# Kernel optimization log

Hardware: AMD Instinct MI355X
Metric: run time of the kernel (lower is better)

## Reference

```python
import jax, jax.numpy as jnp
import numpy as np
from jax import lax

LAP = jnp.array([[1.0, 2.0, 1.0], [2.0, -12.0, 2.0], [1.0, 2.0, 1.0]], jnp.float32)
SOBEL_X = jnp.array([[-1.0, 0.0, 1.0], [-2.0, 0.0, 2.0], [-1.0, 0.0, 1.0]], jnp.float32)

GENE_SIZE = 3
UPDATE_RATE = 0.5
LEAKY_SLOPE = 0.01  # torch leaky_relu default


def _depthwise3x3_circular(x, k):
    # x: [B,C,H,W], k: [3,3]; circular pad then depthwise conv with same kernel per channel
    b, c, h, w = x.shape
    xp = jnp.pad(x, ((0, 0), (0, 0), (1, 1), (1, 1)), mode='wrap')
    kern = jnp.broadcast_to(k, (c, 1, 3, 3))
    return lax.conv_general_dilated(
        xp, kern, window_strides=(1, 1), padding='VALID',
        dimension_numbers=('NCHW', 'OIHW', 'NCHW'), feature_group_count=c)


def setup_inputs() -> dict:
    key = jax.random.key(0)
    k1, k2, k3, k4, k5 = jax.random.split(key, 5)
    chn, hidden_n, gene_size = 12, 128, 3
    perc_n = 3 * chn  # 36
    b, h, w = 16, 256, 256
    return {
        'x': jax.random.normal(k1, (b, chn, h, w), jnp.float32),
        'rand': jax.random.uniform(k2, (b, 1, h, w), jnp.float32),
        'w1_w': jax.random.normal(k3, (hidden_n, perc_n), jnp.float32) * 0.1,
        'w1_b': jax.random.normal(k4, (hidden_n,), jnp.float32) * 0.1,
        'w2_w': jax.random.normal(k5, (chn - gene_size, hidden_n), jnp.float32) * 0.1,
    }


def reference(x, rand, w1_w, w1_b, w2_w):
    b, c, h, w = x.shape
    gene = x[:, -GENE_SIZE:]
    # perception: ident (=x) and laplacian interleaved per channel, then gradient norm
    gx = _depthwise3x3_circular(x, SOBEL_X)
    gy = _depthwise3x3_circular(x, SOBEL_X.T)
    lap_x = _depthwise3x3_circular(x, LAP)
    state_lap = jnp.stack([x, lap_x], axis=2).reshape(b, 2 * c, h, w)  # [x0,lap0,x1,lap1,...]
    gradnorm = jnp.sqrt(gx * gx + gy * gy + 1e-8)
    perc = jnp.concatenate([state_lap, gradnorm], axis=1)  # [B, 3C, H, W]
    # 1x1 conv MLP
    y = jnp.einsum('bchw,oc->bohw', perc, w1_w) + w1_b[None, :, None, None]
    y = jax.nn.leaky_relu(y, LEAKY_SLOPE)
    y = jnp.einsum('bchw,oc->bohw', y, w2_w)  # [B, C-gene, H, W]
    # stochastic update mask
    update_mask = jnp.floor(rand + UPDATE_RATE)  # [B,1,H,W]
    # alive mask: 3x3 max pool (torch pads with -inf) on channel 3
    pool = lax.reduce_window(x[:, 3], -jnp.inf, lax.max,
                             (1, 3, 3), (1, 1, 1), [(0, 0), (1, 1), (1, 1)])
    life = (pool > 0.1)[:, None].astype(x.dtype)  # [B,1,H,W]
    x_new = x[:, :c - GENE_SIZE] + y * update_mask * life
    return jnp.concatenate([x_new, gene], axis=1)
```

## Files before the change

kernel.cpp:

```cpp
#include <hip/hip_runtime.h>
#include <hip/hip_bf16.h>
#include <math.h>

#define CHN  12
#define H    256
#define W    256
#define HID  128
#define OUTC 9
#define PSTR 56
#define YSTR 72

typedef __attribute__((ext_vector_type(4))) float    f32x4;
typedef __attribute__((ext_vector_type(8))) short    s16x8;
typedef __attribute__((ext_vector_type(4))) unsigned u32x4;
typedef __attribute__((ext_vector_type(8))) __bf16   bf16x8;

#define MFMA16x16x32(a, b, c) \
    __builtin_amdgcn_mfma_f32_16x16x32_bf16(__builtin_bit_cast(bf16x8, (a)), \
                                            __builtin_bit_cast(bf16x8, (b)), (c), 0, 0, 0)

static __device__ __forceinline__ unsigned short bfbits(float f) {
    __hip_bfloat16 h = __float2bfloat16(f);
    return __builtin_bit_cast(unsigned short, h);
}
static __device__ __forceinline__ float bits2f(unsigned short u) {
    __hip_bfloat16 h = __builtin_bit_cast(__hip_bfloat16, u);
    return __bfloat162float(h);
}
static __device__ __forceinline__ unsigned rna(float f) {
    return __builtin_bit_cast(unsigned, f) + 0x8000u;
}
static __device__ __forceinline__ unsigned pack2(unsigned uodd, unsigned ueven) {
    return __builtin_amdgcn_perm(uodd, ueven, 0x07060302u);
}
static __device__ __forceinline__ float fast_sqrtf(float x) {
    float r;
    asm("v_sqrt_f32 %0, %1" : "=v"(r) : "v"(x));
    return r;
}

__global__ void prep_weights(const float* __restrict__ w1w, const float* __restrict__ w1b,
                             const float* __restrict__ w2w, unsigned short* __restrict__ wsbuf)
{
    const int t = threadIdx.x;
    const int l = t & 63;
    const int grp = t >> 6;
    const int row = l & 15;
    const int g4 = l >> 4;
    unsigned short* wsa1 = wsbuf;
    unsigned short* wsa2 = wsbuf + 16 * 64 * 8;

    for (int mf = grp; mf < 16; mf += 4) {
        int m = mf >> 1, f = mf & 1;
        int hid = m * 16 + row;
        for (int j = 0; j < 8; ++j) {
            int s = f * 32 + g4 * 8 + j;
            unsigned short v = 0;
            if (s < 36)       v = bfbits(w1w[hid * 36 + s]);
            else if (s < 48)  v = bfbits(w1w[hid * 36 + 2 * (s - 36) + 1]);
            else if (s == 48) v = bfbits(w1b[hid]);
            wsa1[(mf * 64 + l) * 8 + j] = v;
        }
    }
    {
        int kb = grp;
        for (int j = 0; j < 8; ++j) {
            float wv = (row < OUTC) ? w2w[row * HID + kb * 32 + g4 * 8 + j] : 0.f;
            wsa2[(kb * 64 + l) * 8 + j] = bfbits(wv);
        }
    }
}

__global__ __launch_bounds__(256, 3) void nca_main(
    const float* __restrict__ x, const float* __restrict__ rnd,
    const unsigned short* __restrict__ wsbuf, float* __restrict__ out)
{
    union SMem {
        struct { float2 csdd[CHN][W]; float prrow[W]; } s;
        unsigned short perc[W][PSTR];
    };
    __shared__ SMem sm;
    __shared__ unsigned short y1h[4][16][YSTR];

    const int t = threadIdx.x;
    const int orig = ((blockIdx.x & 7) << 9) | (blockIdx.x >> 3);
    const int h = orig & (H - 1);
    const int b = orig >> 8;
    const int hm = (h + H - 1) & (H - 1);
    const int hp = (h + 1) & (H - 1);
    const float* xb = x + (size_t)b * CHN * H * W;

    float xc[CHN], csr[CHN], ddr[CHN];
    const float maskraw = rnd[((size_t)b * H + h) * W + t];
    #pragma unroll
    for (int c = 0; c < CHN; ++c) {
        const float* xp = xb + (size_t)c * H * W;
        float v0 = xp[hm * W + t];
        float v1 = xp[h  * W + t];
        float v2 = xp[hp * W + t];
        xc[c] = v1;
        float cs = fmaf(2.f, v1, v0) + v2;
        float dd = v2 - v0;
        csr[c] = cs; ddr[c] = dd;
        sm.s.csdd[c][t] = make_float2(cs, dd);
        if (c == 3) {
            float cm = v1;
            if (h > 0)     cm = fmaxf(cm, v0);
            if (h < H - 1) cm = fmaxf(cm, v2);
            sm.s.prrow[t] = cm;
        }
    }
    __syncthreads();

    const int wm = (t + W - 1) & (W - 1);
    const int wp = (t + 1) & (W - 1);
    float perc[36];
    #pragma unroll
    for (int c = 0; c < CHN; ++c) {
        float2 vm = sm.s.csdd[c][wm];
        float2 vp = sm.s.csdd[c][wp];
        float gx  = vp.x - vm.x;
        float gy  = fmaf(2.f, ddr[c], vm.y) + vp.y;
        float lap = fmaf(2.f, csr[c], vm.x + vp.x) - 16.f * xc[c];
        perc[2 * c]     = xc[c];
        perc[2 * c + 1] = lap;
        perc[24 + c]    = fast_sqrtf(fmaf(gx, gx, gy * gy) + 1e-8f);
    }
    float scale_reg;
    {
        float pool = sm.s.prrow[t];
        if (t > 0)     pool = fmaxf(pool, sm.s.prrow[wm]);
        if (t < W - 1) pool = fmaxf(pool, sm.s.prrow[wp]);
        scale_reg = (pool > 0.1f && maskraw >= 0.5f) ? 1.f : 0.f;
    }
    const float gene0 = xc[9], gene1 = xc[10], gene2 = xc[11];
    __syncthreads();

    {
        unsigned u[48];
        #pragma unroll
        for (int s = 0; s < 36; ++s) u[s] = rna(perc[s]);
        #pragma unroll
        for (int k = 0; k < 12; ++k) {
            float hif = __builtin_bit_cast(float, u[2 * k + 1] & 0xFFFF0000u);
            u[36 + k] = rna(perc[2 * k + 1] - hif);
        }
        unsigned short* prow = &sm.perc[t][0];
        #pragma unroll
        for (int g = 0; g < 6; ++g) {
            u32x4 v;
            #pragma unroll
            for (int j = 0; j < 4; ++j)
                v[j] = pack2(u[8 * g + 2 * j + 1], u[8 * g + 2 * j]);
            *(u32x4*)&prow[g * 8] = v;
        }
    }

    const int l = t & 63;
    const int wv = t >> 6;
    const int p16 = l & 15;
    const int g4 = l >> 4;
    const s16x8* A1 = (const s16x8*)wsbuf;
    const s16x8* A2 = A1 + 16 * 64;

    s16x8 a1f[16];
    #pragma unroll
    for (int mf = 0; mf < 16; ++mf) a1f[mf] = A1[mf * 64 + l];
    s16x8 a2[4];
    #pragma unroll
    for (int kb = 0; kb < 4; ++kb) a2[kb] = A2[kb * 64 + l];

    s16x8 bhi_c;
    #pragma unroll
    for (int j = 0; j < 8; ++j) bhi_c[j] = 0;
    if (g4 == 2) bhi_c[0] = (short)0x3F80;

    #pragma unroll 1
    for (int pt = 0; pt < 4; ++pt) {
        const int p = wv * 64 + pt * 16 + p16;
        const unsigned short* prow = &sm.perc[p][0];
        s16x8 blo = *(const s16x8*)&prow[g4 * 8];
        s16x8 bhi;
        if (g4 < 2) bhi = *(const s16x8*)&prow[(4 + g4) * 8];
        else        bhi = bhi_c;

        unsigned short* ybase = &y1h[wv][p16][0];
        f32x4 acc2 = {0.f, 0.f, 0.f, 0.f};

        #pragma unroll
        for (int hh = 0; hh < 2; ++hh) {
            f32x4 acc[4];
            #pragma unroll
            for (int m2 = 0; m2 < 4; ++m2) { acc[m2][0] = 0.f; acc[m2][1] = 0.f; acc[m2][2] = 0.f; acc[m2][3] = 0.f; }
            #pragma unroll
            for (int m2 = 0; m2 < 4; ++m2) {
                acc[m2] = MFMA16x16x32(a1f[(hh * 4 + m2) * 2],     blo, acc[m2]);
                acc[m2] = MFMA16x16x32(a1f[(hh * 4 + m2) * 2 + 1], bhi, acc[m2]);
            }
            #pragma unroll
            for (int m2 = 0; m2 < 4; ++m2) {
                float w0 = fmaxf(acc[m2][0], 0.01f * acc[m2][0]);
                float w1 = fmaxf(acc[m2][1], 0.01f * acc[m2][1]);
                float w2 = fmaxf(acc[m2][2], 0.01f * acc[m2][2]);
                float w3 = fmaxf(acc[m2][3], 0.01f * acc[m2][3]);
                unsigned lo = pack2(rna(w1), rna(w0));
                unsigned hi = pack2(rna(w3), rna(w2));
                *(uint2*)(ybase + (2 * m2 + (g4 >> 1)) * 8 + (g4 & 1) * 4) = make_uint2(lo, hi);
            }
            #pragma unroll
            for (int kb2 = 0; kb2 < 2; ++kb2) {
                u32x4 b2 = *(const u32x4*)(ybase + (kb2 * 4 + g4) * 8);
                acc2 = MFMA16x16x32(a2[hh * 2 + kb2], b2, acc2);
            }
        }

        const float sc = __shfl(scale_reg, pt * 16 + p16, 64);
        const size_t pixbase = (size_t)b * CHN * H * W + (size_t)h * W + p;
        #pragma unroll
        for (int r = 0; r < 4; ++r) {
            int o = g4 * 4 + r;
            if (o < OUTC) {
                float xhi = bits2f((unsigned short)blo[2 * r]);
                out[pixbase + (size_t)o * H * W] = fmaf(acc2[r], sc, xhi);
            }
        }
    }

    {
        size_t gidx = ((size_t)b * CHN + 9) * H * W + (size_t)h * W + t;
        out[gidx]                     = gene0;
        out[gidx + (size_t)H * W]     = gene1;
        out[gidx + 2 * (size_t)H * W] = gene2;
    }
}

extern "C" void kernel_launch(void* const* d_in, const int* in_sizes, int n_in,
                              void* d_out, int out_size, void* d_ws, size_t ws_size,
                              hipStream_t stream) {
    const float* x   = (const float*)d_in[0];
    const float* rnd = (const float*)d_in[1];
    const float* w1w = (const float*)d_in[2];
    const float* w1b = (const float*)d_in[3];
    const float* w2w = (const float*)d_in[4];
    float* out = (float*)d_out;
    unsigned short* ws = (unsigned short*)d_ws;

    prep_weights<<<dim3(1), dim3(256), 0, stream>>>(w1w, w1b, w2w, ws);
    nca_main<<<dim3(16 * 256), dim3(256), 0, stream>>>(x, rnd, ws, out);
}
```

Baseline: 54.37 us.

## Fold leaky ReLU into second MFMA via abs decomposition with split weights

Rewrites leaky_relu(y) as 0.505*y + 0.495*|y|. The second layer now runs two MFMAs, one on the raw bf16 hidden values and one on their sign-cleared copies, against prescaled weight copies. This removes the per-element max/mul VALU work on the hidden activations but doubles the second-layer MFMA count and adds register pressure for the extra weight fragments. Rounding differs slightly because the bf16 weights are scaled separately.

```diff
diff --git a/kernel.cpp b/kernel.cpp
--- a/kernel.cpp
+++ b/kernel.cpp
@@ -47,8 +47,9 @@
     const int grp = t >> 6;
     const int row = l & 15;
     const int g4 = l >> 4;
-    unsigned short* wsa1 = wsbuf;
-    unsigned short* wsa2 = wsbuf + 16 * 64 * 8;
+    unsigned short* wsa1  = wsbuf;
+    unsigned short* wsa2p = wsbuf + 16 * 64 * 8;
+    unsigned short* wsa2n = wsa2p + 4 * 64 * 8;
 
     for (int mf = grp; mf < 16; mf += 4) {
         int m = mf >> 1, f = mf & 1;
@@ -66,7 +67,8 @@
         int kb = grp;
         for (int j = 0; j < 8; ++j) {
             float wv = (row < OUTC) ? w2w[row * HID + kb * 32 + g4 * 8 + j] : 0.f;
-            wsa2[(kb * 64 + l) * 8 + j] = bfbits(wv);
+            wsa2p[(kb * 64 + l) * 8 + j] = bfbits(0.505f * wv);
+            wsa2n[(kb * 64 + l) * 8 + j] = bfbits(0.495f * wv);
         }
     }
 }
@@ -160,20 +162,23 @@
     const int wv = t >> 6;
     const int p16 = l & 15;
     const int g4 = l >> 4;
-    const s16x8* A1 = (const s16x8*)wsbuf;
-    const s16x8* A2 = A1 + 16 * 64;
+    const s16x8* A1  = (const s16x8*)wsbuf;
+    const s16x8* A2P = A1 + 16 * 64;
+    const s16x8* A2N = A2P + 4 * 64;
 
     s16x8 a1f[16];
     #pragma unroll
     for (int mf = 0; mf < 16; ++mf) a1f[mf] = A1[mf * 64 + l];
-    s16x8 a2[4];
-    #pragma unroll
-    for (int kb = 0; kb < 4; ++kb) a2[kb] = A2[kb * 64 + l];
+    s16x8 a2p[4], a2n[4];
+    #pragma unroll
+    for (int kb = 0; kb < 4; ++kb) { a2p[kb] = A2P[kb * 64 + l]; a2n[kb] = A2N[kb * 64 + l]; }
 
     s16x8 bhi_c;
     #pragma unroll
     for (int j = 0; j < 8; ++j) bhi_c[j] = 0;
     if (g4 == 2) bhi_c[0] = (short)0x3F80;
+
+    const f32x4 fzero = {0.f, 0.f, 0.f, 0.f};
 
     #pragma unroll 1
     for (int pt = 0; pt < 4; ++pt) {
@@ -185,32 +190,30 @@
         else        bhi = bhi_c;
 
         unsigned short* ybase = &y1h[wv][p16][0];
-        f32x4 acc2 = {0.f, 0.f, 0.f, 0.f};
+        f32x4 acc2 = fzero;
 
         #pragma unroll
         for (int hh = 0; hh < 2; ++hh) {
             f32x4 acc[4];
             #pragma unroll
-            for (int m2 = 0; m2 < 4; ++m2) { acc[m2][0] = 0.f; acc[m2][1] = 0.f; acc[m2][2] = 0.f; acc[m2][3] = 0.f; }
-            #pragma unroll
             for (int m2 = 0; m2 < 4; ++m2) {
-                acc[m2] = MFMA16x16x32(a1f[(hh * 4 + m2) * 2],     blo, acc[m2]);
+                acc[m2] = MFMA16x16x32(a1f[(hh * 4 + m2) * 2],     blo, fzero);
                 acc[m2] = MFMA16x16x32(a1f[(hh * 4 + m2) * 2 + 1], bhi, acc[m2]);
             }
             #pragma unroll
             for (int m2 = 0; m2 < 4; ++m2) {
-                float w0 = fmaxf(acc[m2][0], 0.01f * acc[m2][0]);
-                float w1 = fmaxf(acc[m2][1], 0.01f * acc[m2][1]);
-                float w2 = fmaxf(acc[m2][2], 0.01f * acc[m2][2]);
-                float w3 = fmaxf(acc[m2][3], 0.01f * acc[m2][3]);
-                unsigned lo = pack2(rna(w1), rna(w0));
-                unsigned hi = pack2(rna(w3), rna(w2));
+                unsigned lo = pack2(rna(acc[m2][1]), rna(acc[m2][0]));
+                unsigned hi = pack2(rna(acc[m2][3]), rna(acc[m2][2]));
                 *(uint2*)(ybase + (2 * m2 + (g4 >> 1)) * 8 + (g4 & 1) * 4) = make_uint2(lo, hi);
             }
             #pragma unroll
             for (int kb2 = 0; kb2 < 2; ++kb2) {
-                u32x4 b2 = *(const u32x4*)(ybase + (kb2 * 4 + g4) * 8);
-                acc2 = MFMA16x16x32(a2[hh * 2 + kb2], b2, acc2);
+                u32x4 bv = *(const u32x4*)(ybase + (kb2 * 4 + g4) * 8);
+                u32x4 ba;
+                #pragma unroll
+                for (int j = 0; j < 4; ++j) ba[j] = bv[j] & 0x7FFF7FFFu;
+                acc2 = MFMA16x16x32(a2p[hh * 2 + kb2], bv, acc2);
+                acc2 = MFMA16x16x32(a2n[hh * 2 + kb2], ba, acc2);
             }
         }
 
```

Measured after the change: 55.12 us. No clear change (+1.4%).
